# Performance work log

Measured on AMD Instinct MI355X. Metric: run time of the kernel, lower is better.

## Reference

```python
import jax, jax.numpy as jnp
import numpy as np

N_NODES = 100000
N_EDGES = 3200000
N_GRAPHS = 128
IN_DIM = 4
HID = 64
BN_EPS = 1e-5


def setup_inputs() -> dict:
    key = jax.random.key(0)
    ks = jax.random.split(key, 24)
    x = jax.random.normal(ks[0], (N_NODES, IN_DIM), dtype=jnp.float32)
    edge_index = jax.random.randint(ks[1], (2, N_EDGES), 0, N_NODES, dtype=jnp.int32)
    batch_ids = jnp.sort(jax.random.randint(ks[2], (N_NODES,), 0, N_GRAPHS, dtype=jnp.int32))

    def lin(k, out_d, in_d):
        s = 1.0 / np.sqrt(in_d)
        return jax.random.uniform(k, (out_d, in_d), jnp.float32, -s, s)

    inp = {
        'x': x, 'edge_index': edge_index, 'batch_ids': batch_ids,
        # SAGEConv i: out = lin_l(mean_neighbors) + lin_r(x_self); bias lives in lin_l
        'w1l': lin(ks[3], HID, IN_DIM), 'b1': jnp.zeros((HID,), jnp.float32), 'w1r': lin(ks[4], HID, IN_DIM),
        'bn1_g': jnp.ones((HID,), jnp.float32), 'bn1_b': jnp.zeros((HID,), jnp.float32),
        'w2l': lin(ks[5], HID, HID), 'b2': jnp.zeros((HID,), jnp.float32), 'w2r': lin(ks[6], HID, HID),
        'bn2_g': jnp.ones((HID,), jnp.float32), 'bn2_b': jnp.zeros((HID,), jnp.float32),
        'w3l': lin(ks[7], HID, HID), 'b3': jnp.zeros((HID,), jnp.float32), 'w3r': lin(ks[8], HID, HID),
        'bn3_g': jnp.ones((HID,), jnp.float32), 'bn3_b': jnp.zeros((HID,), jnp.float32),
        'fc1_w': lin(ks[9], 64, HID), 'fc1_b': jnp.zeros((64,), jnp.float32),
        'fc2_w': lin(ks[10], 2, 64), 'fc2_b': jnp.zeros((2,), jnp.float32),
    }
    return inp


def _sage(x, src, dst, deg_inv, wl, bl, wr):
    # mean-aggregate neighbor messages (source -> target), then two small GEMMs
    msum = jax.ops.segment_sum(x[src], dst, num_segments=N_NODES)  # [N, d]
    agg = msum * deg_inv[:, None]
    return agg @ wl.T + bl + x @ wr.T


def _bn(x, g, b):
    # BatchNorm1d in training mode: batch stats over node dim, biased variance
    m = jnp.mean(x, axis=0)
    v = jnp.mean((x - m) ** 2, axis=0)
    return (x - m) * jax.lax.rsqrt(v + BN_EPS) * g + b


def reference(x, edge_index, batch_ids,
              w1l, b1, w1r, bn1_g, bn1_b,
              w2l, b2, w2r, bn2_g, bn2_b,
              w3l, b3, w3r, bn3_g, bn3_b,
              fc1_w, fc1_b, fc2_w, fc2_b):
    src, dst = edge_index[0], edge_index[1]
    deg = jax.ops.segment_sum(jnp.ones((src.shape[0],), x.dtype), dst, num_segments=N_NODES)
    deg_inv = 1.0 / jnp.maximum(deg, 1.0)

    h = jax.nn.relu(_bn(_sage(x, src, dst, deg_inv, w1l, b1, w1r), bn1_g, bn1_b))
    h = jax.nn.relu(_bn(_sage(h, src, dst, deg_inv, w2l, b2, w2r), bn2_g, bn2_b))
    h = jax.nn.relu(_bn(_sage(h, src, dst, deg_inv, w3l, b3, w3r), bn3_g, bn3_b))

    # global_mean_pool over graphs
    gsum = jax.ops.segment_sum(h, batch_ids, num_segments=N_GRAPHS)
    gcnt = jax.ops.segment_sum(jnp.ones((h.shape[0],), h.dtype), batch_ids, num_segments=N_GRAPHS)
    pooled = gsum / jnp.maximum(gcnt, 1.0)[:, None]

    # MLP head (dropout = identity at inference)
    hid = jax.nn.relu(pooled @ fc1_w.T + fc1_b)
    return hid @ fc2_w.T + fc2_b
```

## Files before the change

kernel.cpp:

```cpp
#include <hip/hip_runtime.h>
#include <hip/hip_fp16.h>

#define NN 100000
#define NE 3200000
#define NG 128
#define BN_EPS 1e-5f

#define NBUK 782
#define BSHIFT 7
#define BCAP 6144

#define GRID_SG 1024
#define PBMAX 2048

typedef _Float16 h2v __attribute__((ext_vector_type(2)));

__global__ void __launch_bounds__(512) k_scatter(
    const int* __restrict__ src, const int* __restrict__ dst,
    int* __restrict__ slab_cursor, unsigned int* __restrict__ slab, int E) {
    __shared__ int hist[NBUK + 2];
    __shared__ int cbase[NBUK + 2];
    int tid = threadIdx.x;
    int eBeg = blockIdx.x * 6250;
    int eEnd = min(eBeg + 6250, E);

    for (int t = tid; t < NBUK; t += 512) hist[t] = 0;
    __syncthreads();
    for (int e = eBeg + tid; e < eEnd; e += 512) {
        int b = dst[e] >> BSHIFT;
        atomicAdd(&hist[b], 1);
    }
    __syncthreads();
    for (int t = tid; t < NBUK; t += 512) {
        int c = hist[t];
        cbase[t] = (c > 0) ? atomicAdd(&slab_cursor[t], c) : 0;
    }
    __syncthreads();
    for (int t = tid; t < NBUK; t += 512) hist[t] = 0;
    __syncthreads();
    for (int e = eBeg + tid; e < eEnd; e += 512) {
        int d = dst[e];
        int b = d >> BSHIFT;
        int r = atomicAdd(&hist[b], 1);
        int pos = cbase[b] + r;
        if (pos < BCAP) slab[(size_t)b * BCAP + pos] = ((unsigned)src[e] << BSHIFT) | (unsigned)(d & 127);
    }
}

__global__ void k_bucket_scan(const int* __restrict__ slab_cursor,
                              int* __restrict__ bucket_base, int* __restrict__ row_ptr) {
    __shared__ int sm[1024];
    int t = threadIdx.x;
    int c = (t < NBUK) ? min(slab_cursor[t], BCAP) : 0;
    sm[t] = c;
    __syncthreads();
    for (int off = 1; off < 1024; off <<= 1) {
        int add = (t >= off) ? sm[t - off] : 0;
        __syncthreads();
        sm[t] += add;
        __syncthreads();
    }
    if (t < NBUK) {
        bucket_base[t] = sm[t] - c;
        if (t == NBUK - 1) row_ptr[NN] = sm[t];
    }
}

__global__ void __launch_bounds__(512) k_bucket_csr(
    const unsigned int* __restrict__ slab, const int* __restrict__ slab_cursor,
    const int* __restrict__ bucket_base, int* __restrict__ row_ptr,
    float* __restrict__ deg_inv, int* __restrict__ csr_src,
    const float* __restrict__ x, const float* __restrict__ w1l,
    const float* __restrict__ b1, const float* __restrict__ w1r,
    float* __restrict__ h_pre, float* __restrict__ part) {
    __shared__ int lds_csr[BCAP];
    __shared__ int sdeg[128];
    __shared__ int sscan[128];
    __shared__ int slcur[128];
    __shared__ float swl[256], swr[256], sb1[64];
    __shared__ float ssum[64], ssq[64];
    int tid = threadIdx.x;
    int b = blockIdx.x;
    int lo = b << BSHIFT;
    int cnt = min(slab_cursor[b], BCAP);
    const unsigned int* sl = slab + (size_t)b * BCAP;

    if (tid < 256) { swl[tid] = w1l[tid]; swr[tid] = w1r[tid]; }
    if (tid < 64)  { sb1[tid] = b1[tid]; ssum[tid] = 0.f; ssq[tid] = 0.f; }
    if (tid < 128) sdeg[tid] = 0;
    __syncthreads();
    for (int k = tid; k < cnt; k += 512) {
        atomicAdd(&sdeg[sl[k] & 127], 1);
    }
    __syncthreads();
    int v = (tid < 128) ? sdeg[tid] : 0;
    if (tid < 128) sscan[tid] = v;
    __syncthreads();
    for (int off = 1; off < 128; off <<= 1) {
        int add = 0;
        if (tid < 128 && tid >= off) add = sscan[tid - off];
        __syncthreads();
        if (tid < 128) sscan[tid] += add;
        __syncthreads();
    }
    int base = bucket_base[b];
    if (tid < 128) {
        int excl = sscan[tid] - v;
        int n = lo + tid;
        if (n < NN) {
            row_ptr[n] = base + excl;
            deg_inv[n] = 1.0f / fmaxf((float)v, 1.0f);
        }
        slcur[tid] = excl;
    }
    __syncthreads();
    for (int k = tid; k < cnt; k += 512) {
        unsigned int p = sl[k];
        int pos = atomicAdd(&slcur[p & 127], 1);
        lds_csr[pos] = (int)(p >> BSHIFT);
    }
    __syncthreads();
    for (int k = tid; k < cnt; k += 512) csr_src[base + k] = lds_csr[k];

    int i = tid >> 2, c = tid & 3;
    int n = lo + i;
    bool valid = (n < NN);
    int dhi = sscan[i];
    int dlo = dhi - sdeg[i];
    const float4* x4 = (const float4*)x;
    float4 acc = make_float4(0.f, 0.f, 0.f, 0.f);
    for (int k = dlo + c; k < dhi; k += 4) {
        int s = lds_csr[k];
        float4 xv = x4[s];
        acc.x += xv.x; acc.y += xv.y; acc.z += xv.z; acc.w += xv.w;
    }
#pragma unroll
    for (int m = 1; m <= 2; m <<= 1) {
        acc.x += __shfl_xor(acc.x, m);
        acc.y += __shfl_xor(acc.y, m);
        acc.z += __shfl_xor(acc.z, m);
        acc.w += __shfl_xor(acc.w, m);
    }
    float dv = 1.0f / fmaxf((float)sdeg[i], 1.0f);
    float ax = acc.x * dv, ay = acc.y * dv, az = acc.z * dv, aw = acc.w * dv;
    float4 xs = valid ? x4[n] : make_float4(0.f, 0.f, 0.f, 0.f);

#pragma unroll
    for (int m4 = 0; m4 < 4; m4++) {
        float4 o = make_float4(0.f, 0.f, 0.f, 0.f);
        float* op = &o.x;
        if (valid) {
#pragma unroll
            for (int t = 0; t < 4; t++) {
                int j = c * 16 + m4 * 4 + t;
                float s = sb1[j];
                s += ax * swl[j * 4 + 0] + ay * swl[j * 4 + 1] + az * swl[j * 4 + 2] + aw * swl[j * 4 + 3];
                s += xs.x * swr[j * 4 + 0] + xs.y * swr[j * 4 + 1] + xs.z * swr[j * 4 + 2] + xs.w * swr[j * 4 + 3];
                op[t] = s;
            }
            ((float4*)h_pre)[(size_t)n * 16 + c * 4 + m4] = o;
        }
        float4 q = make_float4(o.x * o.x, o.y * o.y, o.z * o.z, o.w * o.w);
#pragma unroll
        for (int m = 4; m <= 32; m <<= 1) {
            o.x += __shfl_xor(o.x, m); o.y += __shfl_xor(o.y, m);
            o.z += __shfl_xor(o.z, m); o.w += __shfl_xor(o.w, m);
            q.x += __shfl_xor(q.x, m); q.y += __shfl_xor(q.y, m);
            q.z += __shfl_xor(q.z, m); q.w += __shfl_xor(q.w, m);
        }
        if ((tid & 63) < 4) {
            int jb = c * 16 + m4 * 4;
            atomicAdd(&ssum[jb + 0], o.x); atomicAdd(&ssum[jb + 1], o.y);
            atomicAdd(&ssum[jb + 2], o.z); atomicAdd(&ssum[jb + 3], o.w);
            atomicAdd(&ssq[jb + 0], q.x);  atomicAdd(&ssq[jb + 1], q.y);
            atomicAdd(&ssq[jb + 2], q.z);  atomicAdd(&ssq[jb + 3], q.w);
        }
    }
    __syncthreads();
    if (tid < 64) {
        part[(2 * tid) * PBMAX + blockIdx.x]     = ssum[tid];
        part[(2 * tid + 1) * PBMAX + blockIdx.x] = ssq[tid];
    }
}

__global__ void __launch_bounds__(512, 8) k_sage(
    const __half* __restrict__ h_in, const int* __restrict__ row_ptr,
    const int* __restrict__ csr_src, const float* __restrict__ deg_inv,
    const float* __restrict__ wl, const float* __restrict__ bl,
    const float* __restrict__ wr, float* __restrict__ h_pre,
    float* __restrict__ part) {
    __shared__ h2v wl2s[32][68];
    __shared__ h2v wr2s[32][68];
    __shared__ h2v tAh[32][36];
    __shared__ h2v tXh[32][36];
    __shared__ float ssum[64], ssq[64];
    int tid = threadIdx.x;
    for (int idx = tid; idx < 2048; idx += 512) {
        int j = idx & 63, kk = idx >> 6;
        float2 l = ((const float2*)wl)[j * 32 + kk];
        float2 r = ((const float2*)wr)[j * 32 + kk];
        wl2s[kk][j] = h2v{(_Float16)l.x, (_Float16)l.y};
        wr2s[kk][j] = h2v{(_Float16)r.x, (_Float16)r.y};
    }
    if (tid < 64) { ssum[tid] = 0.f; ssq[tid] = 0.f; }
    __syncthreads();

    int g = tid & 15, ni = tid >> 4;
    const uint2* tbl = (const uint2*)h_in;
    const int ntiles = NN / 32;

    for (int tile = blockIdx.x; tile < ntiles; tile += gridDim.x) {
        int n = tile * 32 + ni;
        float ax = 0.f, ay = 0.f, az = 0.f, aw = 0.f;
        int r0 = row_ptr[n], r1 = row_ptr[n + 1];
        int e = r0;
        for (; e + 8 <= r1; e += 8) {
            int s0 = csr_src[e],     s1 = csr_src[e + 1], s2 = csr_src[e + 2], s3 = csr_src[e + 3];
            int s4 = csr_src[e + 4], s5 = csr_src[e + 5], s6 = csr_src[e + 6], s7 = csr_src[e + 7];
            uint2 v0 = tbl[(size_t)s0 * 16 + g];
            uint2 v1 = tbl[(size_t)s1 * 16 + g];
            uint2 v2 = tbl[(size_t)s2 * 16 + g];
            uint2 v3 = tbl[(size_t)s3 * 16 + g];
            uint2 v4 = tbl[(size_t)s4 * 16 + g];
            uint2 v5 = tbl[(size_t)s5 * 16 + g];
            uint2 v6 = tbl[(size_t)s6 * 16 + g];
            uint2 v7 = tbl[(size_t)s7 * 16 + g];
            float2 f;
            f = __half22float2(*(__half2*)&v0.x); ax += f.x; ay += f.y;
            f = __half22float2(*(__half2*)&v0.y); az += f.x; aw += f.y;
            f = __half22float2(*(__half2*)&v1.x); ax += f.x; ay += f.y;
            f = __half22float2(*(__half2*)&v1.y); az += f.x; aw += f.y;
            f = __half22float2(*(__half2*)&v2.x); ax += f.x; ay += f.y;
            f = __half22float2(*(__half2*)&v2.y); az += f.x; aw += f.y;
            f = __half22float2(*(__half2*)&v3.x); ax += f.x; ay += f.y;
            f = __half22float2(*(__half2*)&v3.y); az += f.x; aw += f.y;
            f = __half22float2(*(__half2*)&v4.x); ax += f.x; ay += f.y;
            f = __half22float2(*(__half2*)&v4.y); az += f.x; aw += f.y;
            f = __half22float2(*(__half2*)&v5.x); ax += f.x; ay += f.y;
            f = __half22float2(*(__half2*)&v5.y); az += f.x; aw += f.y;
            f = __half22float2(*(__half2*)&v6.x); ax += f.x; ay += f.y;
            f = __half22float2(*(__half2*)&v6.y); az += f.x; aw += f.y;
            f = __half22float2(*(__half2*)&v7.x); ax += f.x; ay += f.y;
            f = __half22float2(*(__half2*)&v7.y); az += f.x; aw += f.y;
        }
        for (; e < r1; ++e) {
            int s = csr_src[e];
            uint2 v = tbl[(size_t)s * 16 + g];
            float2 f;
            f = __half22float2(*(__half2*)&v.x); ax += f.x; ay += f.y;
            f = __half22float2(*(__half2*)&v.y); az += f.x; aw += f.y;
        }
        float di = deg_inv[n];
        uint2 rs = tbl[(size_t)n * 16 + g];
        ax *= di; ay *= di; az *= di; aw *= di;
        tAh[ni][2 * g]     = h2v{(_Float16)ax, (_Float16)ay};
        tAh[ni][2 * g + 1] = h2v{(_Float16)az, (_Float16)aw};
        *(uint2*)&tXh[ni][2 * g] = rs;
        __syncthreads();

        float4 o = ((const float4*)bl)[g];
#pragma unroll 4
        for (int kk = 0; kk < 32; kk++) {
            h2v a2 = tAh[ni][kk];
            h2v x2 = tXh[ni][kk];
            h2v l0 = wl2s[kk][4 * g + 0], l1 = wl2s[kk][4 * g + 1];
            h2v l2 = wl2s[kk][4 * g + 2], l3 = wl2s[kk][4 * g + 3];
            h2v r0v = wr2s[kk][4 * g + 0], r1v = wr2s[kk][4 * g + 1];
            h2v r2v = wr2s[kk][4 * g + 2], r3v = wr2s[kk][4 * g + 3];
#if __has_builtin(__builtin_amdgcn_fdot2)
            o.x = __builtin_amdgcn_fdot2(a2, l0, o.x, false);
            o.y = __builtin_amdgcn_fdot2(a2, l1, o.y, false);
            o.z = __builtin_amdgcn_fdot2(a2, l2, o.z, false);
            o.w = __builtin_amdgcn_fdot2(a2, l3, o.w, false);
            o.x = __builtin_amdgcn_fdot2(x2, r0v, o.x, false);
            o.y = __builtin_amdgcn_fdot2(x2, r1v, o.y, false);
            o.z = __builtin_amdgcn_fdot2(x2, r2v, o.z, false);
            o.w = __builtin_amdgcn_fdot2(x2, r3v, o.w, false);
#else
            float b0 = (float)a2.x, b1 = (float)a2.y, x0 = (float)x2.x, x1 = (float)x2.y;
            o.x += b0 * (float)l0.x + b1 * (float)l0.y + x0 * (float)r0v.x + x1 * (float)r0v.y;
            o.y += b0 * (float)l1.x + b1 * (float)l1.y + x0 * (float)r1v.x + x1 * (float)r1v.y;
            o.z += b0 * (float)l2.x + b1 * (float)l2.y + x0 * (float)r2v.x + x1 * (float)r2v.y;
            o.w += b0 * (float)l3.x + b1 * (float)l3.y + x0 * (float)r3v.x + x1 * (float)r3v.y;
#endif
        }
        ((float4*)h_pre)[(size_t)n * 16 + g] = o;

        float4 qv = make_float4(o.x * o.x, o.y * o.y, o.z * o.z, o.w * o.w);
#pragma unroll
        for (int m = 16; m <= 32; m <<= 1) {
            o.x += __shfl_xor(o.x, m); o.y += __shfl_xor(o.y, m);
            o.z += __shfl_xor(o.z, m); o.w += __shfl_xor(o.w, m);
            qv.x += __shfl_xor(qv.x, m); qv.y += __shfl_xor(qv.y, m);
            qv.z += __shfl_xor(qv.z, m); qv.w += __shfl_xor(qv.w, m);
        }
        if ((tid & 48) == 0) {
            atomicAdd(&ssum[4 * g + 0], o.x); atomicAdd(&ssum[4 * g + 1], o.y);
            atomicAdd(&ssum[4 * g + 2], o.z); atomicAdd(&ssum[4 * g + 3], o.w);
            atomicAdd(&ssq[4 * g + 0], qv.x);  atomicAdd(&ssq[4 * g + 1], qv.y);
            atomicAdd(&ssq[4 * g + 2], qv.z);  atomicAdd(&ssq[4 * g + 3], qv.w);
        }
        __syncthreads();
    }
    if (tid < 64) {
        part[(2 * tid) * PBMAX + blockIdx.x]     = ssum[tid];
        part[(2 * tid + 1) * PBMAX + blockIdx.x] = ssq[tid];
    }
}

__global__ void k_reduce_sb(const float* __restrict__ part, int PB,
                            const float* __restrict__ gamma, const float* __restrict__ beta,
                            float* __restrict__ sbv, int N) {
    int c = blockIdx.x;
    float s = 0.f, q = 0.f;
    for (int b = threadIdx.x; b < PB; b += 256) {
        s += part[(2 * c) * PBMAX + b];
        q += part[(2 * c + 1) * PBMAX + b];
    }
    __shared__ float rs[256], rq[256];
    rs[threadIdx.x] = s;
    rq[threadIdx.x] = q;
    __syncthreads();
    for (int off = 128; off > 0; off >>= 1) {
        if (threadIdx.x < off) {
            rs[threadIdx.x] += rs[threadIdx.x + off];
            rq[threadIdx.x] += rq[threadIdx.x + off];
        }
        __syncthreads();
    }
    if (threadIdx.x == 0) {
        float m = rs[0] / (float)N;
        float var = rq[0] / (float)N - m * m;
        float sc = gamma[c] * rsqrtf(var + BN_EPS);
        sbv[c]      = sc;
        sbv[64 + c] = beta[c] - m * sc;
    }
}

__global__ void k_bnrelu_h(const float* __restrict__ h_pre, const float* __restrict__ sbv,
                           __half* __restrict__ h, int N) {
    __shared__ float s_sc[64], s_bi[64];
    if (threadIdx.x < 64) {
        s_sc[threadIdx.x] = sbv[threadIdx.x];
        s_bi[threadIdx.x] = sbv[64 + threadIdx.x];
    }
    __syncthreads();
    int total = N * 16;
    for (int i = blockIdx.x * blockDim.x + threadIdx.x; i < total; i += gridDim.x * blockDim.x) {
        float4 v = ((const float4*)h_pre)[i];
        int c4 = (i & 15) * 4;
        v.x = fmaxf(v.x * s_sc[c4 + 0] + s_bi[c4 + 0], 0.f);
        v.y = fmaxf(v.y * s_sc[c4 + 1] + s_bi[c4 + 1], 0.f);
        v.z = fmaxf(v.z * s_sc[c4 + 2] + s_bi[c4 + 2], 0.f);
        v.w = fmaxf(v.w * s_sc[c4 + 3] + s_bi[c4 + 3], 0.f);
        __half2 p0 = __floats2half2_rn(v.x, v.y);
        __half2 p1 = __floats2half2_rn(v.z, v.w);
        uint2 o;
        o.x = *(unsigned int*)&p0;
        o.y = *(unsigned int*)&p1;
        ((uint2*)h)[i] = o;
    }
}

__global__ void k_poolhead(const __half* __restrict__ h, const int* __restrict__ batch,
                           const float* __restrict__ fc1w, const float* __restrict__ fc1b,
                           const float* __restrict__ fc2w, const float* __restrict__ fc2b,
                           float* __restrict__ out, int N) {
    int gph = blockIdx.x;
    int lo = 0, hi = N;
    while (lo < hi) { int mid = (lo + hi) >> 1; if (batch[mid] < gph) lo = mid + 1; else hi = mid; }
    int start = lo;
    hi = N;
    while (lo < hi) { int mid = (lo + hi) >> 1; if (batch[mid] < gph + 1) lo = mid + 1; else hi = mid; }
    int end = lo;

    int c = threadIdx.x & 63, w = threadIdx.x >> 6;
    float s = 0.f;
    for (int r = start + w; r < end; r += 4) s += __half2float(h[(size_t)r * 64 + c]);
    __shared__ float sm[256];
    __shared__ float pl[64], hid[64];
    sm[threadIdx.x] = s;
    __syncthreads();
    if (threadIdx.x < 64) {
        float t = sm[c] + sm[64 + c] + sm[128 + c] + sm[192 + c];
        pl[c] = t / fmaxf((float)(end - start), 1.0f);
    }
    __syncthreads();
    if (threadIdx.x < 64) {
        int j = threadIdx.x;
        float v = fc1b[j];
        for (int k = 0; k < 64; k++) v += pl[k] * fc1w[j * 64 + k];
        hid[j] = fmaxf(v, 0.f);
    }
    __syncthreads();
    if (threadIdx.x < 2) {
        int j = threadIdx.x;
        float o = fc2b[j];
        for (int k = 0; k < 64; k++) o += hid[k] * fc2w[j * 64 + k];
        out[gph * 2 + j] = o;
    }
}

extern "C" void kernel_launch(void* const* d_in, const int* in_sizes, int n_in,
                              void* d_out, int out_size, void* d_ws, size_t ws_size,
                              hipStream_t stream) {
    const float* x    = (const float*)d_in[0];
    const int* ei     = (const int*)d_in[1];
    const int* batch  = (const int*)d_in[2];
    const float* w1l  = (const float*)d_in[3];
    const float* b1   = (const float*)d_in[4];
    const float* w1r  = (const float*)d_in[5];
    const float* bn1g = (const float*)d_in[6];
    const float* bn1b = (const float*)d_in[7];
    const float* w2l  = (const float*)d_in[8];
    const float* b2   = (const float*)d_in[9];
    const float* w2r  = (const float*)d_in[10];
    const float* bn2g = (const float*)d_in[11];
    const float* bn2b = (const float*)d_in[12];
    const float* w3l  = (const float*)d_in[13];
    const float* b3   = (const float*)d_in[14];
    const float* w3r  = (const float*)d_in[15];
    const float* bn3g = (const float*)d_in[16];
    const float* bn3b = (const float*)d_in[17];
    const float* fc1w = (const float*)d_in[18];
    const float* fc1b = (const float*)d_in[19];
    const float* fc2w = (const float*)d_in[20];
    const float* fc2b = (const float*)d_in[21];
    float* out = (float*)d_out;

    const int N = NN, E = NE;
    const int* srcp = ei;
    const int* dstp = ei + E;

    char* ws = (char*)d_ws;
    size_t off = 0;
    auto alloc = [&](size_t bytes) -> char* {
        char* p = ws + off;
        off += (bytes + 255) & ~(size_t)255;
        return p;
    };
    int* csr_src       = (int*)alloc(sizeof(int) * E);
    float* hB          = (float*)alloc(sizeof(float) * N * 64);
    __half* hH         = (__half*)alloc(sizeof(__half) * N * 64);
    unsigned int* slab = (unsigned int*)alloc(sizeof(unsigned int) * (size_t)NBUK * BCAP);
    int* slab_cursor   = (int*)alloc(sizeof(int) * NBUK);
    int* bucket_base   = (int*)alloc(sizeof(int) * NBUK);
    int* row_ptr       = (int*)alloc(sizeof(int) * (N + 1));
    float* deg_inv     = (float*)alloc(sizeof(float) * N);
    float* part        = (float*)alloc(sizeof(float) * 128 * PBMAX);
    float* sbv         = (float*)alloc(sizeof(float) * 128);

    hipMemsetAsync(slab_cursor, 0, sizeof(int) * NBUK, stream);

    k_scatter<<<512, 512, 0, stream>>>(srcp, dstp, slab_cursor, slab, E);
    k_bucket_scan<<<1, 1024, 0, stream>>>(slab_cursor, bucket_base, row_ptr);
    k_bucket_csr<<<NBUK, 512, 0, stream>>>(slab, slab_cursor, bucket_base, row_ptr, deg_inv,
                                           csr_src, x, w1l, b1, w1r, hB, part);
    k_reduce_sb<<<64, 256, 0, stream>>>(part, NBUK, bn1g, bn1b, sbv, N);
    k_bnrelu_h<<<1024, 256, 0, stream>>>(hB, sbv, hH, N);

    k_sage<<<GRID_SG, 512, 0, stream>>>(hH, row_ptr, csr_src, deg_inv, w2l, b2, w2r, hB, part);
    k_reduce_sb<<<64, 256, 0, stream>>>(part, GRID_SG, bn2g, bn2b, sbv, N);
    k_bnrelu_h<<<1024, 256, 0, stream>>>(hB, sbv, hH, N);

    k_sage<<<GRID_SG, 512, 0, stream>>>(hH, row_ptr, csr_src, deg_inv, w3l, b3, w3r, hB, part);
    k_reduce_sb<<<64, 256, 0, stream>>>(part, GRID_SG, bn3g, bn3b, sbv, N);
    k_bnrelu_h<<<1024, 256, 0, stream>>>(hB, sbv, hH, N);

    k_poolhead<<<NG, 256, 0, stream>>>(hH, batch, fc1w, fc1b, fc2w, fc2b, out, N);
}
```

Measured before the change: 447.7 us.

## Fuse all pipeline stages into one persistent kernel with grid barriers

Replaces the chain of roughly a dozen kernel launches (scatter, scan, CSR build, sage layers, BN reduce, BN-ReLU, pool head) with a single persistent kernel of 512 blocks. Phases are separated by atomic-counter grid barriers in global memory. The pool head now applies the final BN-ReLU inline from the fp32 buffer instead of running a separate pass. This removes launch gaps and per-kernel ramp-up. In exchange it relies on all 512 blocks being co-resident, since otherwise the spin barrier deadlocks, and the sage layers run with half the previous grid.

```diff
diff --git a/kernel.cpp b/kernel.cpp
--- a/kernel.cpp
+++ b/kernel.cpp
@@ -10,213 +10,124 @@
 #define BSHIFT 7
 #define BCAP 6144
 
-#define GRID_SG 1024
+#define GRID_MB 512
+#define NTHR 512
 #define PBMAX 2048
 
 typedef _Float16 h2v __attribute__((ext_vector_type(2)));
 
-__global__ void __launch_bounds__(512) k_scatter(
-    const int* __restrict__ src, const int* __restrict__ dst,
-    int* __restrict__ slab_cursor, unsigned int* __restrict__ slab, int E) {
-    __shared__ int hist[NBUK + 2];
-    __shared__ int cbase[NBUK + 2];
-    int tid = threadIdx.x;
-    int eBeg = blockIdx.x * 6250;
-    int eEnd = min(eBeg + 6250, E);
-
-    for (int t = tid; t < NBUK; t += 512) hist[t] = 0;
+struct Params {
+    const float* x; const int* src; const int* dst; const int* batch;
+    const float* w1l; const float* b1; const float* w1r; const float* bn1g; const float* bn1b;
+    const float* w2l; const float* b2; const float* w2r; const float* bn2g; const float* bn2b;
+    const float* w3l; const float* b3; const float* w3r; const float* bn3g; const float* bn3b;
+    const float* fc1w; const float* fc1b; const float* fc2w; const float* fc2b;
+    float* out;
+    int* csr_src; float* hB; __half* hH;
+    unsigned int* slab; int* slab_cursor; int* bucket_base; int* row_ptr; float* deg_inv;
+    float* part; float* sbv; int* bar;
+};
+
+struct SmemBK {
+    int lds_csr[BCAP];
+    int sdeg[128]; int sscan[128]; int slcur[128];
+    float swl[256]; float swr[256]; float sb1[64];
+    float ssum[64]; float ssq[64];
+};
+struct SmemSage {
+    h2v wl2s[32][68]; h2v wr2s[32][68];
+    h2v tAh[32][36]; h2v tXh[32][36];
+    float ssum[64]; float ssq[64];
+};
+
+__device__ inline void gsync(int* bar, int slot) {
     __syncthreads();
-    for (int e = eBeg + tid; e < eEnd; e += 512) {
-        int b = dst[e] >> BSHIFT;
-        atomicAdd(&hist[b], 1);
+    if (threadIdx.x == 0) {
+        __hip_atomic_fetch_add(&bar[slot], 1, __ATOMIC_ACQ_REL, __HIP_MEMORY_SCOPE_AGENT);
+        while (__hip_atomic_load(&bar[slot], __ATOMIC_ACQUIRE, __HIP_MEMORY_SCOPE_AGENT) < GRID_MB) {
+            __builtin_amdgcn_s_sleep(2);
+        }
     }
     __syncthreads();
-    for (int t = tid; t < NBUK; t += 512) {
-        int c = hist[t];
-        cbase[t] = (c > 0) ? atomicAdd(&slab_cursor[t], c) : 0;
-    }
+}
+
+
+__device__ inline void reduce_sb_phase(const Params& p, char* smem,
+                                       const float* gamma, const float* beta) {
+    int tid = threadIdx.x, bid = blockIdx.x;
+    if (bid >= 64) return;
+    float* rs = (float*)smem;
+    float* rq = rs + NTHR;
+    int c = bid;
+    float sv = 0.f, qv = 0.f;
+    for (int b = tid; b < GRID_MB; b += NTHR) {
+        sv += p.part[(2 * c) * PBMAX + b];
+        qv += p.part[(2 * c + 1) * PBMAX + b];
+    }
+    rs[tid] = sv; rq[tid] = qv;
     __syncthreads();
-    for (int t = tid; t < NBUK; t += 512) hist[t] = 0;
+    for (int off = NTHR / 2; off > 0; off >>= 1) {
+        if (tid < off) { rs[tid] += rs[tid + off]; rq[tid] += rq[tid + off]; }
+        __syncthreads();
+    }
+    if (tid == 0) {
+        float m = rs[0] / (float)NN;
+        float var = rq[0] / (float)NN - m * m;
+        float sc = gamma[c] * rsqrtf(var + BN_EPS);
+        p.sbv[c] = sc;
+        p.sbv[64 + c] = beta[c] - m * sc;
+    }
+}
+
+__device__ inline void bnrelu_phase(const Params& p, char* smem) {
+    int tid = threadIdx.x, bid = blockIdx.x;
+    float* ssc = (float*)smem;
+    float* sbi = ssc + 64;
+    if (tid < 64) { ssc[tid] = p.sbv[tid]; sbi[tid] = p.sbv[64 + tid]; }
     __syncthreads();
-    for (int e = eBeg + tid; e < eEnd; e += 512) {
-        int d = dst[e];
-        int b = d >> BSHIFT;
-        int r = atomicAdd(&hist[b], 1);
-        int pos = cbase[b] + r;
-        if (pos < BCAP) slab[(size_t)b * BCAP + pos] = ((unsigned)src[e] << BSHIFT) | (unsigned)(d & 127);
-    }
-}
-
-__global__ void k_bucket_scan(const int* __restrict__ slab_cursor,
-                              int* __restrict__ bucket_base, int* __restrict__ row_ptr) {
-    __shared__ int sm[1024];
-    int t = threadIdx.x;
-    int c = (t < NBUK) ? min(slab_cursor[t], BCAP) : 0;
-    sm[t] = c;
-    __syncthreads();
-    for (int off = 1; off < 1024; off <<= 1) {
-        int add = (t >= off) ? sm[t - off] : 0;
-        __syncthreads();
-        sm[t] += add;
-        __syncthreads();
-    }
-    if (t < NBUK) {
-        bucket_base[t] = sm[t] - c;
-        if (t == NBUK - 1) row_ptr[NN] = sm[t];
-    }
-}
-
-__global__ void __launch_bounds__(512) k_bucket_csr(
-    const unsigned int* __restrict__ slab, const int* __restrict__ slab_cursor,
-    const int* __restrict__ bucket_base, int* __restrict__ row_ptr,
-    float* __restrict__ deg_inv, int* __restrict__ csr_src,
-    const float* __restrict__ x, const float* __restrict__ w1l,
-    const float* __restrict__ b1, const float* __restrict__ w1r,
-    float* __restrict__ h_pre, float* __restrict__ part) {
-    __shared__ int lds_csr[BCAP];
-    __shared__ int sdeg[128];
-    __shared__ int sscan[128];
-    __shared__ int slcur[128];
-    __shared__ float swl[256], swr[256], sb1[64];
-    __shared__ float ssum[64], ssq[64];
-    int tid = threadIdx.x;
-    int b = blockIdx.x;
-    int lo = b << BSHIFT;
-    int cnt = min(slab_cursor[b], BCAP);
-    const unsigned int* sl = slab + (size_t)b * BCAP;
-
-    if (tid < 256) { swl[tid] = w1l[tid]; swr[tid] = w1r[tid]; }
-    if (tid < 64)  { sb1[tid] = b1[tid]; ssum[tid] = 0.f; ssq[tid] = 0.f; }
-    if (tid < 128) sdeg[tid] = 0;
-    __syncthreads();
-    for (int k = tid; k < cnt; k += 512) {
-        atomicAdd(&sdeg[sl[k] & 127], 1);
-    }
-    __syncthreads();
-    int v = (tid < 128) ? sdeg[tid] : 0;
-    if (tid < 128) sscan[tid] = v;
-    __syncthreads();
-    for (int off = 1; off < 128; off <<= 1) {
-        int add = 0;
-        if (tid < 128 && tid >= off) add = sscan[tid - off];
-        __syncthreads();
-        if (tid < 128) sscan[tid] += add;
-        __syncthreads();
-    }
-    int base = bucket_base[b];
-    if (tid < 128) {
-        int excl = sscan[tid] - v;
-        int n = lo + tid;
-        if (n < NN) {
-            row_ptr[n] = base + excl;
-            deg_inv[n] = 1.0f / fmaxf((float)v, 1.0f);
-        }
-        slcur[tid] = excl;
-    }
-    __syncthreads();
-    for (int k = tid; k < cnt; k += 512) {
-        unsigned int p = sl[k];
-        int pos = atomicAdd(&slcur[p & 127], 1);
-        lds_csr[pos] = (int)(p >> BSHIFT);
-    }
-    __syncthreads();
-    for (int k = tid; k < cnt; k += 512) csr_src[base + k] = lds_csr[k];
-
-    int i = tid >> 2, c = tid & 3;
-    int n = lo + i;
-    bool valid = (n < NN);
-    int dhi = sscan[i];
-    int dlo = dhi - sdeg[i];
-    const float4* x4 = (const float4*)x;
-    float4 acc = make_float4(0.f, 0.f, 0.f, 0.f);
-    for (int k = dlo + c; k < dhi; k += 4) {
-        int s = lds_csr[k];
-        float4 xv = x4[s];
-        acc.x += xv.x; acc.y += xv.y; acc.z += xv.z; acc.w += xv.w;
-    }
-#pragma unroll
-    for (int m = 1; m <= 2; m <<= 1) {
-        acc.x += __shfl_xor(acc.x, m);
-        acc.y += __shfl_xor(acc.y, m);
-        acc.z += __shfl_xor(acc.z, m);
-        acc.w += __shfl_xor(acc.w, m);
-    }
-    float dv = 1.0f / fmaxf((float)sdeg[i], 1.0f);
-    float ax = acc.x * dv, ay = acc.y * dv, az = acc.z * dv, aw = acc.w * dv;
-    float4 xs = valid ? x4[n] : make_float4(0.f, 0.f, 0.f, 0.f);
-
-#pragma unroll
-    for (int m4 = 0; m4 < 4; m4++) {
-        float4 o = make_float4(0.f, 0.f, 0.f, 0.f);
-        float* op = &o.x;
-        if (valid) {
-#pragma unroll
-            for (int t = 0; t < 4; t++) {
-                int j = c * 16 + m4 * 4 + t;
-                float s = sb1[j];
-                s += ax * swl[j * 4 + 0] + ay * swl[j * 4 + 1] + az * swl[j * 4 + 2] + aw * swl[j * 4 + 3];
-                s += xs.x * swr[j * 4 + 0] + xs.y * swr[j * 4 + 1] + xs.z * swr[j * 4 + 2] + xs.w * swr[j * 4 + 3];
-                op[t] = s;
-            }
-            ((float4*)h_pre)[(size_t)n * 16 + c * 4 + m4] = o;
-        }
-        float4 q = make_float4(o.x * o.x, o.y * o.y, o.z * o.z, o.w * o.w);
-#pragma unroll
-        for (int m = 4; m <= 32; m <<= 1) {
-            o.x += __shfl_xor(o.x, m); o.y += __shfl_xor(o.y, m);
-            o.z += __shfl_xor(o.z, m); o.w += __shfl_xor(o.w, m);
-            q.x += __shfl_xor(q.x, m); q.y += __shfl_xor(q.y, m);
-            q.z += __shfl_xor(q.z, m); q.w += __shfl_xor(q.w, m);
-        }
-        if ((tid & 63) < 4) {
-            int jb = c * 16 + m4 * 4;
-            atomicAdd(&ssum[jb + 0], o.x); atomicAdd(&ssum[jb + 1], o.y);
-            atomicAdd(&ssum[jb + 2], o.z); atomicAdd(&ssum[jb + 3], o.w);
-            atomicAdd(&ssq[jb + 0], q.x);  atomicAdd(&ssq[jb + 1], q.y);
-            atomicAdd(&ssq[jb + 2], q.z);  atomicAdd(&ssq[jb + 3], q.w);
-        }
-    }
-    __syncthreads();
-    if (tid < 64) {
-        part[(2 * tid) * PBMAX + blockIdx.x]     = ssum[tid];
-        part[(2 * tid + 1) * PBMAX + blockIdx.x] = ssq[tid];
-    }
-}
-
-__global__ void __launch_bounds__(512, 8) k_sage(
-    const __half* __restrict__ h_in, const int* __restrict__ row_ptr,
-    const int* __restrict__ csr_src, const float* __restrict__ deg_inv,
-    const float* __restrict__ wl, const float* __restrict__ bl,
-    const float* __restrict__ wr, float* __restrict__ h_pre,
-    float* __restrict__ part) {
-    __shared__ h2v wl2s[32][68];
-    __shared__ h2v wr2s[32][68];
-    __shared__ h2v tAh[32][36];
-    __shared__ h2v tXh[32][36];
-    __shared__ float ssum[64], ssq[64];
-    int tid = threadIdx.x;
-    for (int idx = tid; idx < 2048; idx += 512) {
+    int total = NN * 16;
+    for (int i = bid * NTHR + tid; i < total; i += GRID_MB * NTHR) {
+        float4 v = ((const float4*)p.hB)[i];
+        int c4 = (i & 15) * 4;
+        v.x = fmaxf(v.x * ssc[c4 + 0] + sbi[c4 + 0], 0.f);
+        v.y = fmaxf(v.y * ssc[c4 + 1] + sbi[c4 + 1], 0.f);
+        v.z = fmaxf(v.z * ssc[c4 + 2] + sbi[c4 + 2], 0.f);
+        v.w = fmaxf(v.w * ssc[c4 + 3] + sbi[c4 + 3], 0.f);
+        __half2 p0 = __floats2half2_rn(v.x, v.y);
+        __half2 p1 = __floats2half2_rn(v.z, v.w);
+        uint2 o;
+        o.x = *(unsigned int*)&p0;
+        o.y = *(unsigned int*)&p1;
+        ((uint2*)p.hH)[i] = o;
+    }
+}
+
+__device__ inline void sage_phase(const Params& p, char* smem,
+                                  const float* wl, const float* bl, const float* wr) {
+    SmemSage* s = (SmemSage*)smem;
+    int tid = threadIdx.x, bid = blockIdx.x;
+    for (int idx = tid; idx < 2048; idx += NTHR) {
         int j = idx & 63, kk = idx >> 6;
         float2 l = ((const float2*)wl)[j * 32 + kk];
         float2 r = ((const float2*)wr)[j * 32 + kk];
-        wl2s[kk][j] = h2v{(_Float16)l.x, (_Float16)l.y};
-        wr2s[kk][j] = h2v{(_Float16)r.x, (_Float16)r.y};
-    }
-    if (tid < 64) { ssum[tid] = 0.f; ssq[tid] = 0.f; }
+        s->wl2s[kk][j] = h2v{(_Float16)l.x, (_Float16)l.y};
+        s->wr2s[kk][j] = h2v{(_Float16)r.x, (_Float16)r.y};
+    }
+    if (tid < 64) { s->ssum[tid] = 0.f; s->ssq[tid] = 0.f; }
     __syncthreads();
 
     int g = tid & 15, ni = tid >> 4;
-    const uint2* tbl = (const uint2*)h_in;
+    const uint2* tbl = (const uint2*)p.hH;
     const int ntiles = NN / 32;
 
-    for (int tile = blockIdx.x; tile < ntiles; tile += gridDim.x) {
+    for (int tile = bid; tile < ntiles; tile += GRID_MB) {
         int n = tile * 32 + ni;
         float ax = 0.f, ay = 0.f, az = 0.f, aw = 0.f;
-        int r0 = row_ptr[n], r1 = row_ptr[n + 1];
+        int r0 = p.row_ptr[n], r1 = p.row_ptr[n + 1];
         int e = r0;
         for (; e + 8 <= r1; e += 8) {
-            int s0 = csr_src[e],     s1 = csr_src[e + 1], s2 = csr_src[e + 2], s3 = csr_src[e + 3];
-            int s4 = csr_src[e + 4], s5 = csr_src[e + 5], s6 = csr_src[e + 6], s7 = csr_src[e + 7];
+            int s0 = p.csr_src[e],     s1 = p.csr_src[e + 1], s2 = p.csr_src[e + 2], s3 = p.csr_src[e + 3];
+            int s4 = p.csr_src[e + 4], s5 = p.csr_src[e + 5], s6 = p.csr_src[e + 6], s7 = p.csr_src[e + 7];
             uint2 v0 = tbl[(size_t)s0 * 16 + g];
             uint2 v1 = tbl[(size_t)s1 * 16 + g];
             uint2 v2 = tbl[(size_t)s2 * 16 + g];
@@ -244,29 +155,29 @@
             f = __half22float2(*(__half2*)&v7.y); az += f.x; aw += f.y;
         }
         for (; e < r1; ++e) {
-            int s = csr_src[e];
-            uint2 v = tbl[(size_t)s * 16 + g];
+            int sx = p.csr_src[e];
+            uint2 v = tbl[(size_t)sx * 16 + g];
             float2 f;
             f = __half22float2(*(__half2*)&v.x); ax += f.x; ay += f.y;
             f = __half22float2(*(__half2*)&v.y); az += f.x; aw += f.y;
         }
-        float di = deg_inv[n];
-        uint2 rs = tbl[(size_t)n * 16 + g];
+        float di = p.deg_inv[n];
+        uint2 rsv = tbl[(size_t)n * 16 + g];
         ax *= di; ay *= di; az *= di; aw *= di;
-        tAh[ni][2 * g]     = h2v{(_Float16)ax, (_Float16)ay};
-        tAh[ni][2 * g + 1] = h2v{(_Float16)az, (_Float16)aw};
-        *(uint2*)&tXh[ni][2 * g] = rs;
+        s->tAh[ni][2 * g]     = h2v{(_Float16)ax, (_Float16)ay};
+        s->tAh[ni][2 * g + 1] = h2v{(_Float16)az, (_Float16)aw};
+        *(uint2*)&s->tXh[ni][2 * g] = rsv;
         __syncthreads();
 
         float4 o = ((const float4*)bl)[g];
 #pragma unroll 4
         for (int kk = 0; kk < 32; kk++) {
-            h2v a2 = tAh[ni][kk];
-            h2v x2 = tXh[ni][kk];
-            h2v l0 = wl2s[kk][4 * g + 0], l1 = wl2s[kk][4 * g + 1];
-            h2v l2 = wl2s[kk][4 * g + 2], l3 = wl2s[kk][4 * g + 3];
-            h2v r0v = wr2s[kk][4 * g + 0], r1v = wr2s[kk][4 * g + 1];
-            h2v r2v = wr2s[kk][4 * g + 2], r3v = wr2s[kk][4 * g + 3];
+            h2v a2 = s->tAh[ni][kk];
+            h2v x2 = s->tXh[ni][kk];
+            h2v l0 = s->wl2s[kk][4 * g + 0], l1 = s->wl2s[kk][4 * g + 1];
+            h2v l2 = s->wl2s[kk][4 * g + 2], l3 = s->wl2s[kk][4 * g + 3];
+            h2v r0v = s->wr2s[kk][4 * g + 0], r1v = s->wr2s[kk][4 * g + 1];
+            h2v r2v = s->wr2s[kk][4 * g + 2], r3v = s->wr2s[kk][4 * g + 3];
 #if __has_builtin(__builtin_amdgcn_fdot2)
             o.x = __builtin_amdgcn_fdot2(a2, l0, o.x, false);
             o.y = __builtin_amdgcn_fdot2(a2, l1, o.y, false);
@@ -284,7 +195,7 @@
             o.w += b0 * (float)l3.x + b1 * (float)l3.y + x0 * (float)r3v.x + x1 * (float)r3v.y;
 #endif
         }
-        ((float4*)h_pre)[(size_t)n * 16 + g] = o;
+        ((float4*)p.hB)[(size_t)n * 16 + g] = o;
 
         float4 qv = make_float4(o.x * o.x, o.y * o.y, o.z * o.z, o.w * o.w);
 #pragma unroll
@@ -295,177 +206,287 @@
             qv.z += __shfl_xor(qv.z, m); qv.w += __shfl_xor(qv.w, m);
         }
         if ((tid & 48) == 0) {
-            atomicAdd(&ssum[4 * g + 0], o.x); atomicAdd(&ssum[4 * g + 1], o.y);
-            atomicAdd(&ssum[4 * g + 2], o.z); atomicAdd(&ssum[4 * g + 3], o.w);
-            atomicAdd(&ssq[4 * g + 0], qv.x);  atomicAdd(&ssq[4 * g + 1], qv.y);
-            atomicAdd(&ssq[4 * g + 2], qv.z);  atomicAdd(&ssq[4 * g + 3], qv.w);
+            atomicAdd(&s->ssum[4 * g + 0], o.x); atomicAdd(&s->ssum[4 * g + 1], o.y);
+            atomicAdd(&s->ssum[4 * g + 2], o.z); atomicAdd(&s->ssum[4 * g + 3], o.w);
+            atomicAdd(&s->ssq[4 * g + 0], qv.x);  atomicAdd(&s->ssq[4 * g + 1], qv.y);
+            atomicAdd(&s->ssq[4 * g + 2], qv.z);  atomicAdd(&s->ssq[4 * g + 3], qv.w);
         }
         __syncthreads();
     }
     if (tid < 64) {
-        part[(2 * tid) * PBMAX + blockIdx.x]     = ssum[tid];
-        part[(2 * tid + 1) * PBMAX + blockIdx.x] = ssq[tid];
-    }
-}
-
-__global__ void k_reduce_sb(const float* __restrict__ part, int PB,
-                            const float* __restrict__ gamma, const float* __restrict__ beta,
-                            float* __restrict__ sbv, int N) {
-    int c = blockIdx.x;
-    float s = 0.f, q = 0.f;
-    for (int b = threadIdx.x; b < PB; b += 256) {
-        s += part[(2 * c) * PBMAX + b];
-        q += part[(2 * c + 1) * PBMAX + b];
-    }
-    __shared__ float rs[256], rq[256];
-    rs[threadIdx.x] = s;
-    rq[threadIdx.x] = q;
-    __syncthreads();
-    for (int off = 128; off > 0; off >>= 1) {
-        if (threadIdx.x < off) {
-            rs[threadIdx.x] += rs[threadIdx.x + off];
-            rq[threadIdx.x] += rq[threadIdx.x + off];
-        }
-        __syncthreads();
-    }
-    if (threadIdx.x == 0) {
-        float m = rs[0] / (float)N;
-        float var = rq[0] / (float)N - m * m;
-        float sc = gamma[c] * rsqrtf(var + BN_EPS);
-        sbv[c]      = sc;
-        sbv[64 + c] = beta[c] - m * sc;
-    }
-}
-
-__global__ void k_bnrelu_h(const float* __restrict__ h_pre, const float* __restrict__ sbv,
-                           __half* __restrict__ h, int N) {
-    __shared__ float s_sc[64], s_bi[64];
-    if (threadIdx.x < 64) {
-        s_sc[threadIdx.x] = sbv[threadIdx.x];
-        s_bi[threadIdx.x] = sbv[64 + threadIdx.x];
-    }
-    __syncthreads();
-    int total = N * 16;
-    for (int i = blockIdx.x * blockDim.x + threadIdx.x; i < total; i += gridDim.x * blockDim.x) {
-        float4 v = ((const float4*)h_pre)[i];
-        int c4 = (i & 15) * 4;
-        v.x = fmaxf(v.x * s_sc[c4 + 0] + s_bi[c4 + 0], 0.f);
-        v.y = fmaxf(v.y * s_sc[c4 + 1] + s_bi[c4 + 1], 0.f);
-        v.z = fmaxf(v.z * s_sc[c4 + 2] + s_bi[c4 + 2], 0.f);
-        v.w = fmaxf(v.w * s_sc[c4 + 3] + s_bi[c4 + 3], 0.f);
-        __half2 p0 = __floats2half2_rn(v.x, v.y);
-        __half2 p1 = __floats2half2_rn(v.z, v.w);
-        uint2 o;
-        o.x = *(unsigned int*)&p0;
-        o.y = *(unsigned int*)&p1;
-        ((uint2*)h)[i] = o;
-    }
-}
-
-__global__ void k_poolhead(const __half* __restrict__ h, const int* __restrict__ batch,
-                           const float* __restrict__ fc1w, const float* __restrict__ fc1b,
-                           const float* __restrict__ fc2w, const float* __restrict__ fc2b,
-                           float* __restrict__ out, int N) {
-    int gph = blockIdx.x;
-    int lo = 0, hi = N;
-    while (lo < hi) { int mid = (lo + hi) >> 1; if (batch[mid] < gph) lo = mid + 1; else hi = mid; }
-    int start = lo;
-    hi = N;
-    while (lo < hi) { int mid = (lo + hi) >> 1; if (batch[mid] < gph + 1) lo = mid + 1; else hi = mid; }
-    int end = lo;
-
-    int c = threadIdx.x & 63, w = threadIdx.x >> 6;
-    float s = 0.f;
-    for (int r = start + w; r < end; r += 4) s += __half2float(h[(size_t)r * 64 + c]);
-    __shared__ float sm[256];
-    __shared__ float pl[64], hid[64];
-    sm[threadIdx.x] = s;
-    __syncthreads();
-    if (threadIdx.x < 64) {
-        float t = sm[c] + sm[64 + c] + sm[128 + c] + sm[192 + c];
-        pl[c] = t / fmaxf((float)(end - start), 1.0f);
-    }
-    __syncthreads();
-    if (threadIdx.x < 64) {
-        int j = threadIdx.x;
-        float v = fc1b[j];
-        for (int k = 0; k < 64; k++) v += pl[k] * fc1w[j * 64 + k];
-        hid[j] = fmaxf(v, 0.f);
-    }
-    __syncthreads();
-    if (threadIdx.x < 2) {
-        int j = threadIdx.x;
-        float o = fc2b[j];
-        for (int k = 0; k < 64; k++) o += hid[k] * fc2w[j * 64 + k];
-        out[gph * 2 + j] = o;
+        p.part[(2 * tid) * PBMAX + bid]     = s->ssum[tid];
+        p.part[(2 * tid + 1) * PBMAX + bid] = s->ssq[tid];
+    }
+}
+
+
+__global__ void __launch_bounds__(NTHR, 4) k_mega(Params p) {
+    int tid = threadIdx.x, bid = blockIdx.x;
+    __shared__ __align__(16) char smem[28928];
+    int slot = 0;
+
+    {
+        int gi = bid * NTHR + tid;
+        if (gi < NBUK) p.slab_cursor[gi] = 0;
+    }
+    gsync(p.bar, slot++);
+
+    {
+        int* hist  = (int*)smem;
+        int* cbase = hist + NBUK;
+        const int EPB = (NE + GRID_MB - 1) / GRID_MB;
+        int eBeg = bid * EPB;
+        int eEnd = min(eBeg + EPB, NE);
+        for (int t = tid; t < NBUK; t += NTHR) hist[t] = 0;
+        __syncthreads();
+        for (int e = eBeg + tid; e < eEnd; e += NTHR)
+            atomicAdd(&hist[p.dst[e] >> BSHIFT], 1);
+        __syncthreads();
+        for (int t = tid; t < NBUK; t += NTHR) {
+            int c = hist[t];
+            cbase[t] = (c > 0) ? atomicAdd(&p.slab_cursor[t], c) : 0;
+        }
+        __syncthreads();
+        for (int t = tid; t < NBUK; t += NTHR) hist[t] = 0;
+        __syncthreads();
+        for (int e = eBeg + tid; e < eEnd; e += NTHR) {
+            int d = p.dst[e];
+            int b = d >> BSHIFT;
+            int r = atomicAdd(&hist[b], 1);
+            int pos = cbase[b] + r;
+            if (pos < BCAP)
+                p.slab[(size_t)b * BCAP + pos] = ((unsigned)p.src[e] << BSHIFT) | (unsigned)(d & 127);
+        }
+    }
+    gsync(p.bar, slot++);
+
+    if (bid == 0) {
+        int* sm = (int*)smem;
+        int i1 = tid + NTHR;
+        int c0 = (tid < NBUK) ? min(p.slab_cursor[tid], BCAP) : 0;
+        int c1 = (i1 < NBUK) ? min(p.slab_cursor[i1], BCAP) : 0;
+        sm[tid] = c0; sm[i1] = c1;
+        __syncthreads();
+        for (int off = 1; off < 1024; off <<= 1) {
+            int a0 = (tid >= off) ? sm[tid - off] : 0;
+            int a1 = (i1 >= off) ? sm[i1 - off] : 0;
+            __syncthreads();
+            sm[tid] += a0; sm[i1] += a1;
+            __syncthreads();
+        }
+        if (tid < NBUK) p.bucket_base[tid] = sm[tid] - c0;
+        if (i1 < NBUK) p.bucket_base[i1] = sm[i1] - c1;
+        if (tid == 0) p.row_ptr[NN] = sm[NBUK - 1];
+    }
+    gsync(p.bar, slot++);
+
+    {
+        SmemBK* s = (SmemBK*)smem;
+        if (tid < 256) { s->swl[tid] = p.w1l[tid]; s->swr[tid] = p.w1r[tid]; }
+        if (tid < 64)  { s->sb1[tid] = p.b1[tid]; s->ssum[tid] = 0.f; s->ssq[tid] = 0.f; }
+        for (int b = bid; b < NBUK; b += GRID_MB) {
+            int lo = b << BSHIFT;
+            int cnt = min(p.slab_cursor[b], BCAP);
+            const unsigned int* sl = p.slab + (size_t)b * BCAP;
+            if (tid < 128) s->sdeg[tid] = 0;
+            __syncthreads();
+            for (int k = tid; k < cnt; k += NTHR)
+                atomicAdd(&s->sdeg[sl[k] & 127], 1);
+            __syncthreads();
+            int v = (tid < 128) ? s->sdeg[tid] : 0;
+            if (tid < 128) s->sscan[tid] = v;
+            __syncthreads();
+            for (int off = 1; off < 128; off <<= 1) {
+                int add = 0;
+                if (tid < 128 && tid >= off) add = s->sscan[tid - off];
+                __syncthreads();
+                if (tid < 128) s->sscan[tid] += add;
+                __syncthreads();
+            }
+            int base = p.bucket_base[b];
+            if (tid < 128) {
+                int excl = s->sscan[tid] - v;
+                int n = lo + tid;
+                if (n < NN) {
+                    p.row_ptr[n] = base + excl;
+                    p.deg_inv[n] = 1.0f / fmaxf((float)v, 1.0f);
+                }
+                s->slcur[tid] = excl;
+            }
+            __syncthreads();
+            for (int k = tid; k < cnt; k += NTHR) {
+                unsigned int pk = sl[k];
+                int pos = atomicAdd(&s->slcur[pk & 127], 1);
+                s->lds_csr[pos] = (int)(pk >> BSHIFT);
+            }
+            __syncthreads();
+            for (int k = tid; k < cnt; k += NTHR) p.csr_src[base + k] = s->lds_csr[k];
+
+            int i = tid >> 2, c = tid & 3;
+            int n = lo + i;
+            bool valid = (n < NN);
+            int dhi = s->sscan[i];
+            int dlo2 = dhi - s->sdeg[i];
+            const float4* x4 = (const float4*)p.x;
+            float4 acc = make_float4(0.f, 0.f, 0.f, 0.f);
+            for (int k = dlo2 + c; k < dhi; k += 4) {
+                int sx = s->lds_csr[k];
+                float4 xv = x4[sx];
+                acc.x += xv.x; acc.y += xv.y; acc.z += xv.z; acc.w += xv.w;
+            }
+#pragma unroll
+            for (int m = 1; m <= 2; m <<= 1) {
+                acc.x += __shfl_xor(acc.x, m);
+                acc.y += __shfl_xor(acc.y, m);
+                acc.z += __shfl_xor(acc.z, m);
+                acc.w += __shfl_xor(acc.w, m);
+            }
+            float dv = 1.0f / fmaxf((float)s->sdeg[i], 1.0f);
+            float ax = acc.x * dv, ay = acc.y * dv, az = acc.z * dv, aw = acc.w * dv;
+            float4 xs = valid ? x4[n] : make_float4(0.f, 0.f, 0.f, 0.f);
+#pragma unroll
+            for (int m4 = 0; m4 < 4; m4++) {
+                float4 o = make_float4(0.f, 0.f, 0.f, 0.f);
+                float* op = &o.x;
+                if (valid) {
+#pragma unroll
+                    for (int t = 0; t < 4; t++) {
+                        int j = c * 16 + m4 * 4 + t;
+                        float sv = s->sb1[j];
+                        sv += ax * s->swl[j * 4 + 0] + ay * s->swl[j * 4 + 1] + az * s->swl[j * 4 + 2] + aw * s->swl[j * 4 + 3];
+                        sv += xs.x * s->swr[j * 4 + 0] + xs.y * s->swr[j * 4 + 1] + xs.z * s->swr[j * 4 + 2] + xs.w * s->swr[j * 4 + 3];
+                        op[t] = sv;
+                    }
+                    ((float4*)p.hB)[(size_t)n * 16 + c * 4 + m4] = o;
+                }
+                float4 q = make_float4(o.x * o.x, o.y * o.y, o.z * o.z, o.w * o.w);
+#pragma unroll
+                for (int m = 4; m <= 32; m <<= 1) {
+                    o.x += __shfl_xor(o.x, m); o.y += __shfl_xor(o.y, m);
+                    o.z += __shfl_xor(o.z, m); o.w += __shfl_xor(o.w, m);
+                    q.x += __shfl_xor(q.x, m); q.y += __shfl_xor(q.y, m);
+                    q.z += __shfl_xor(q.z, m); q.w += __shfl_xor(q.w, m);
+                }
+                if ((tid & 63) < 4) {
+                    int jb = c * 16 + m4 * 4;
+                    atomicAdd(&s->ssum[jb + 0], o.x); atomicAdd(&s->ssum[jb + 1], o.y);
+                    atomicAdd(&s->ssum[jb + 2], o.z); atomicAdd(&s->ssum[jb + 3], o.w);
+                    atomicAdd(&s->ssq[jb + 0], q.x);  atomicAdd(&s->ssq[jb + 1], q.y);
+                    atomicAdd(&s->ssq[jb + 2], q.z);  atomicAdd(&s->ssq[jb + 3], q.w);
+                }
+            }
+            __syncthreads();
+        }
+        __syncthreads();
+        if (tid < 64) {
+            p.part[(2 * tid) * PBMAX + bid]     = s->ssum[tid];
+            p.part[(2 * tid + 1) * PBMAX + bid] = s->ssq[tid];
+        }
+    }
+    gsync(p.bar, slot++);
+
+    reduce_sb_phase(p, smem, p.bn1g, p.bn1b);
+    gsync(p.bar, slot++);
+    bnrelu_phase(p, smem);
+    gsync(p.bar, slot++);
+
+    sage_phase(p, smem, p.w2l, p.b2, p.w2r);
+    gsync(p.bar, slot++);
+    reduce_sb_phase(p, smem, p.bn2g, p.bn2b);
+    gsync(p.bar, slot++);
+    bnrelu_phase(p, smem);
+    gsync(p.bar, slot++);
+
+    sage_phase(p, smem, p.w3l, p.b3, p.w3r);
+    gsync(p.bar, slot++);
+    reduce_sb_phase(p, smem, p.bn3g, p.bn3b);
+    gsync(p.bar, slot++);
+
+    if (bid < NG) {
+        float* ssc = (float*)smem;
+        float* sbi = ssc + 64;
+        float* smR = sbi + 64;
+        float* pl  = smR + NTHR;
+        float* hid = pl + 64;
+        if (tid < 64) { ssc[tid] = p.sbv[tid]; sbi[tid] = p.sbv[64 + tid]; }
+        __syncthreads();
+        int gph = bid;
+        int lo = 0, hi = NN;
+        while (lo < hi) { int mid = (lo + hi) >> 1; if (p.batch[mid] < gph) lo = mid + 1; else hi = mid; }
+        int start = lo;
+        hi = NN;
+        while (lo < hi) { int mid = (lo + hi) >> 1; if (p.batch[mid] < gph + 1) lo = mid + 1; else hi = mid; }
+        int end = lo;
+
+        int c = tid & 63, w = tid >> 6;
+        float sacc = 0.f;
+        for (int r = start + w; r < end; r += 8) {
+            float v = p.hB[(size_t)r * 64 + c];
+            sacc += fmaxf(v * ssc[c] + sbi[c], 0.f);
+        }
+        smR[tid] = sacc;
+        __syncthreads();
+        if (tid < 64) {
+            float t2 = 0.f;
+#pragma unroll
+            for (int k = 0; k < 8; k++) t2 += smR[k * 64 + c];
+            pl[c] = t2 / fmaxf((float)(end - start), 1.0f);
+        }
+        __syncthreads();
+        if (tid < 64) {
+            int j = tid;
+            float v = p.fc1b[j];
+            for (int k = 0; k < 64; k++) v += pl[k] * p.fc1w[j * 64 + k];
+            hid[j] = fmaxf(v, 0.f);
+        }
+        __syncthreads();
+        if (tid < 2) {
+            int j = tid;
+            float o = p.fc2b[j];
+            for (int k = 0; k < 64; k++) o += hid[k] * p.fc2w[j * 64 + k];
+            p.out[gph * 2 + j] = o;
+        }
     }
 }
 
 extern "C" void kernel_launch(void* const* d_in, const int* in_sizes, int n_in,
                               void* d_out, int out_size, void* d_ws, size_t ws_size,
                               hipStream_t stream) {
-    const float* x    = (const float*)d_in[0];
-    const int* ei     = (const int*)d_in[1];
-    const int* batch  = (const int*)d_in[2];
-    const float* w1l  = (const float*)d_in[3];
-    const float* b1   = (const float*)d_in[4];
-    const float* w1r  = (const float*)d_in[5];
-    const float* bn1g = (const float*)d_in[6];
-    const float* bn1b = (const float*)d_in[7];
-    const float* w2l  = (const float*)d_in[8];
-    const float* b2   = (const float*)d_in[9];
-    const float* w2r  = (const float*)d_in[10];
-    const float* bn2g = (const float*)d_in[11];
-    const float* bn2b = (const float*)d_in[12];
-    const float* w3l  = (const float*)d_in[13];
-    const float* b3   = (const float*)d_in[14];
-    const float* w3r  = (const float*)d_in[15];
-    const float* bn3g = (const float*)d_in[16];
-    const float* bn3b = (const float*)d_in[17];
-    const float* fc1w = (const float*)d_in[18];
-    const float* fc1b = (const float*)d_in[19];
-    const float* fc2w = (const float*)d_in[20];
-    const float* fc2b = (const float*)d_in[21];
-    float* out = (float*)d_out;
-
-    const int N = NN, E = NE;
-    const int* srcp = ei;
-    const int* dstp = ei + E;
+    Params prm;
+    prm.x    = (const float*)d_in[0];
+    const int* ei = (const int*)d_in[1];
+    prm.src  = ei;
+    prm.dst  = ei + NE;
+    prm.batch = (const int*)d_in[2];
+    prm.w1l = (const float*)d_in[3];  prm.b1 = (const float*)d_in[4];  prm.w1r = (const float*)d_in[5];
+    prm.bn1g = (const float*)d_in[6]; prm.bn1b = (const float*)d_in[7];
+    prm.w2l = (const float*)d_in[8];  prm.b2 = (const float*)d_in[9];  prm.w2r = (const float*)d_in[10];
+    prm.bn2g = (const float*)d_in[11]; prm.bn2b = (const float*)d_in[12];
+    prm.w3l = (const float*)d_in[13]; prm.b3 = (const float*)d_in[14]; prm.w3r = (const float*)d_in[15];
+    prm.bn3g = (const float*)d_in[16]; prm.bn3b = (const float*)d_in[17];
+    prm.fc1w = (const float*)d_in[18]; prm.fc1b = (const float*)d_in[19];
+    prm.fc2w = (const float*)d_in[20]; prm.fc2b = (const float*)d_in[21];
+    prm.out = (float*)d_out;
 
     char* ws = (char*)d_ws;
     size_t off = 0;
     auto alloc = [&](size_t bytes) -> char* {
-        char* p = ws + off;
+        char* pp = ws + off;
         off += (bytes + 255) & ~(size_t)255;
-        return p;
+        return pp;
     };
-    int* csr_src       = (int*)alloc(sizeof(int) * E);
-    float* hB          = (float*)alloc(sizeof(float) * N * 64);
-    __half* hH         = (__half*)alloc(sizeof(__half) * N * 64);
-    unsigned int* slab = (unsigned int*)alloc(sizeof(unsigned int) * (size_t)NBUK * BCAP);
-    int* slab_cursor   = (int*)alloc(sizeof(int) * NBUK);
-    int* bucket_base   = (int*)alloc(sizeof(int) * NBUK);
-    int* row_ptr       = (int*)alloc(sizeof(int) * (N + 1));
-    float* deg_inv     = (float*)alloc(sizeof(float) * N);
-    float* part        = (float*)alloc(sizeof(float) * 128 * PBMAX);
-    float* sbv         = (float*)alloc(sizeof(float) * 128);
-
-    hipMemsetAsync(slab_cursor, 0, sizeof(int) * NBUK, stream);
-
-    k_scatter<<<512, 512, 0, stream>>>(srcp, dstp, slab_cursor, slab, E);
-    k_bucket_scan<<<1, 1024, 0, stream>>>(slab_cursor, bucket_base, row_ptr);
-    k_bucket_csr<<<NBUK, 512, 0, stream>>>(slab, slab_cursor, bucket_base, row_ptr, deg_inv,
-                                           csr_src, x, w1l, b1, w1r, hB, part);
-    k_reduce_sb<<<64, 256, 0, stream>>>(part, NBUK, bn1g, bn1b, sbv, N);
-    k_bnrelu_h<<<1024, 256, 0, stream>>>(hB, sbv, hH, N);
-
-    k_sage<<<GRID_SG, 512, 0, stream>>>(hH, row_ptr, csr_src, deg_inv, w2l, b2, w2r, hB, part);
-    k_reduce_sb<<<64, 256, 0, stream>>>(part, GRID_SG, bn2g, bn2b, sbv, N);
-    k_bnrelu_h<<<1024, 256, 0, stream>>>(hB, sbv, hH, N);
-
-    k_sage<<<GRID_SG, 512, 0, stream>>>(hH, row_ptr, csr_src, deg_inv, w3l, b3, w3r, hB, part);
-    k_reduce_sb<<<64, 256, 0, stream>>>(part, GRID_SG, bn3g, bn3b, sbv, N);
-    k_bnrelu_h<<<1024, 256, 0, stream>>>(hB, sbv, hH, N);
-
-    k_poolhead<<<NG, 256, 0, stream>>>(hH, batch, fc1w, fc1b, fc2w, fc2b, out, N);
-}
+    prm.csr_src     = (int*)alloc(sizeof(int) * NE);
+    prm.hB          = (float*)alloc(sizeof(float) * NN * 64);
+    prm.hH          = (__half*)alloc(sizeof(__half) * NN * 64);
+    prm.slab        = (unsigned int*)alloc(sizeof(unsigned int) * (size_t)NBUK * BCAP);
+    prm.slab_cursor = (int*)alloc(sizeof(int) * NBUK);
+    prm.bucket_base = (int*)alloc(sizeof(int) * NBUK);
+    prm.row_ptr     = (int*)alloc(sizeof(int) * (NN + 1));
+    prm.deg_inv     = (float*)alloc(sizeof(float) * NN);
+    prm.part        = (float*)alloc(sizeof(float) * 128 * PBMAX);
+    prm.sbv         = (float*)alloc(sizeof(float) * 128);
+    prm.bar         = (int*)alloc(sizeof(int) * 64);
+
+    hipMemsetAsync(prm.bar, 0, sizeof(int) * 64, stream);
+    k_mega<<<GRID_MB, NTHR, 0, stream>>>(prm);
+}
```

Result: slower. 1.125 ms (+151.4%).
